# Optimization experiments

Hardware: AMD Instinct MI355X
Metric: run time of the kernel (lower is better)

The kernel has to match this reference:

```python
import jax, jax.numpy as jnp
import numpy as np

B, T, D, H = 4, 4096, 2048, 128

def setup_inputs() -> dict:
    key = jax.random.key(0)
    k1, k2, k3, k4 = jax.random.split(key, 4)
    scale = 0.02
    return {
        "x": jax.random.normal(k1, (B, T, D), dtype=jnp.float32),
        "Wq": jax.random.normal(k2, (D, H), dtype=jnp.float32) * scale,
        "Wk": jax.random.normal(k3, (D, H), dtype=jnp.float32) * scale,
        "Wv": jax.random.normal(k4, (D, H), dtype=jnp.float32) * scale,
    }

def reference(x, Wq, Wk, Wv):
    # x: [B,T,D]; projections to [B,T,H]
    q = jnp.einsum('btd,dh->bth', x, Wq)
    k = jnp.einsum('btd,dh->bth', x, Wk)
    v = jnp.einsum('btd,dh->bth', x, Wv)
    scale = 1.0 / jnp.sqrt(jnp.asarray(q.shape[-1], q.dtype))
    scores = jnp.einsum('bth,bsh->bts', q, k) * scale  # [B,T,T]
    t = x.shape[1]
    causal = jnp.tril(jnp.ones((t, t), dtype=bool))
    scores = jnp.where(causal, scores, -jnp.inf)
    weights = jax.nn.softmax(scores, axis=-1)
    # dropout p=0.0 (eval) -> identity
    out = jnp.einsum('bts,bsh->bth', weights, v)
    return out
```

## Files before the change

### kernel.cpp

```cpp
#include <hip/hip_runtime.h>
#include <hip/hip_bf16.h>

#define Bq 4
#define Tq 4096
#define Dq 2048
#define Hq 128
#define Mq (Bq*Tq)
#define CHUNK 16

typedef __attribute__((ext_vector_type(8))) short bf16x8;
typedef __attribute__((ext_vector_type(4))) float f32x4;

static __device__ __forceinline__ short bfbits(float f) {
    union { __hip_bfloat16 h; short s; } u;
    u.h = __float2bfloat16(f);
    return u.s;
}
static __device__ __forceinline__ float bf2f(short s) {
    union { unsigned u; float f; } v;
    v.u = ((unsigned)(unsigned short)s) << 16;
    return v.f;
}
#define WAIT_LDS() __builtin_amdgcn_s_waitcnt(0xC07F)

static __device__ __forceinline__ void gload16(const void* g, void* l) {
    __builtin_amdgcn_global_load_lds(
        (const __attribute__((address_space(1))) unsigned int*)g,
        (__attribute__((address_space(3))) unsigned int*)l, 16, 0, 0);
}

__global__ __launch_bounds__(256, 1) void wt_kernel(
    const float* __restrict__ Wqp,
    const float* __restrict__ Wkp,
    const float* __restrict__ Wvp,
    short* __restrict__ wTg)
{
    __shared__ short trsp[128][136];
    const int kc = blockIdx.x;
    const int w  = blockIdx.y;
    const float* __restrict__ W = (w == 0) ? Wqp : (w == 1) ? Wkp : Wvp;
    const float scale = (w == 0) ? 0.08838834764831843f : 1.0f;
    const int t = threadIdx.x;

    #pragma unroll
    for (int i = 0; i < 16; i++) {
        int idx = t + i * 256;
        int r = idx >> 5, c4 = idx & 31;
        float4 f = *(const float4*)&W[(size_t)(kc * 128 + r) * Hq + c4 * 4];
        trsp[c4 * 4 + 0][r] = bfbits(f.x * scale);
        trsp[c4 * 4 + 1][r] = bfbits(f.y * scale);
        trsp[c4 * 4 + 2][r] = bfbits(f.z * scale);
        trsp[c4 * 4 + 3][r] = bfbits(f.w * scale);
    }
    __syncthreads();
    #pragma unroll
    for (int i = 0; i < 8; i++) {
        int idx = t + i * 256;
        int h = idx >> 4, c8 = idx & 15;
        *(bf16x8*)&wTg[((size_t)w * 128 + h) * Dq + kc * 128 + c8 * 8] =
            *(bf16x8*)&trsp[h][c8 * 8];
    }
}

__global__ __launch_bounds__(512, 2) void qkv_fused_kernel(
    const float* __restrict__ x,
    const short* __restrict__ wTg,
    short* __restrict__ qg,
    short* __restrict__ kg,
    short* __restrict__ vTt)
{
    __shared__ __attribute__((aligned(128))) char smem[131072];

    const int m0   = blockIdx.x * 64;
    const int t    = threadIdx.x;
    const int l    = t & 63;
    const int w    = t >> 6;
    const int l15  = l & 15;
    const int quad = l >> 4;
    const int wm   = (w >> 2) * 32;
    const int wn   = (w & 3) * 96;

    f32x4 o[2][6];
    #pragma unroll
    for (int mf = 0; mf < 2; mf++)
        #pragma unroll
        for (int j = 0; j < 6; j++) o[mf][j] = (f32x4){0.f, 0.f, 0.f, 0.f};

    const short* wsrcb = wTg + (size_t)(w * 48 + (l >> 3)) * Dq
                             + (((l & 7) ^ ((l >> 3) & 7)) << 3);
    const int xr0 = w * 8 + (l >> 4);

    #define QKV_STAGE(it2, buf)                                                  \
        do {                                                                     \
            const int k0_ = (it2) * 64;                                          \
            char* xb_ = smem + (buf) * 65536;                                    \
            char* wb_ = xb_ + 16384;                                             \
            _Pragma("unroll")                                                    \
            for (int j2 = 0; j2 < 2; j2++) {                                     \
                int r_ = xr0 + j2 * 4;                                           \
                int kbs_ = ((l & 15) ^ (r_ & 15)) << 4;                          \
                gload16((const char*)(x + (size_t)(m0 + r_) * Dq + k0_) + kbs_,  \
                        xb_ + (w * 2 + j2) * 1024);                              \
            }                                                                    \
            _Pragma("unroll")                                                    \
            for (int j = 0; j < 6; j++)                                          \
                gload16(wsrcb + (size_t)j * 8 * Dq + k0_,                        \
                        wb_ + (w * 6 + j) * 1024);                               \
        } while (0)

    QKV_STAGE(0, 0);
    QKV_STAGE(1, 1);

    #pragma unroll 2
    for (int it = 0; it < 32; ++it) {
        if (it < 31) asm volatile("s_waitcnt vmcnt(8)" ::: "memory");
        else         asm volatile("s_waitcnt vmcnt(0)" ::: "memory");
        __builtin_amdgcn_s_barrier();
        __builtin_amdgcn_sched_barrier(0);

        const char* xb = smem + (it & 1) * 65536;
        const char* wb = xb + 16384;
        #pragma unroll
        for (int kk = 0; kk < 2; kk++) {
            bf16x8 a[2];
            #pragma unroll
            for (int mf = 0; mf < 2; mf++) {
                int rm = wm + mf * 16 + l15;
                int sh = (rm & 15) << 4;
                int kb = kk * 128 + quad * 32;
                f32x4 f0 = *(const f32x4*)(xb + rm * 256 + ((kb     ) ^ sh));
                f32x4 f1 = *(const f32x4*)(xb + rm * 256 + ((kb + 16) ^ sh));
                bf16x8 af;
                af[0] = bfbits(f0[0]); af[1] = bfbits(f0[1]);
                af[2] = bfbits(f0[2]); af[3] = bfbits(f0[3]);
                af[4] = bfbits(f1[0]); af[5] = bfbits(f1[1]);
                af[6] = bfbits(f1[2]); af[7] = bfbits(f1[3]);
                a[mf] = af;
            }
            bf16x8 bw[6];
            #pragma unroll
            for (int j = 0; j < 6; j++) {
                int n = wn + j * 16 + l15;
                bw[j] = *(const bf16x8*)(wb + n * 128 +
                        ((kk * 64 + quad * 16) ^ ((n & 7) << 4)));
            }
            #pragma unroll
            for (int mf = 0; mf < 2; mf++)
                #pragma unroll
                for (int j = 0; j < 6; j++)
                    o[mf][j] = __builtin_amdgcn_mfma_f32_16x16x32_bf16(
                        a[mf], bw[j], o[mf][j], 0, 0, 0);
        }

        __builtin_amdgcn_s_barrier();
        __builtin_amdgcn_sched_barrier(0);
        if (it < 30) QKV_STAGE(it + 2, it & 1);
    }
    #undef QKV_STAGE

    {
        short (*e64)[264] = (short(*)[264])smem;
        #pragma unroll
        for (int mf = 0; mf < 2; mf++)
            #pragma unroll
            for (int j = 0; j < 6; j++) {
                int n0 = wn + j * 16;
                if (n0 < 256) {
                    #pragma unroll
                    for (int reg = 0; reg < 4; reg++)
                        e64[wm + mf * 16 + quad * 4 + reg][n0 + l15] = bfbits(o[mf][j][reg]);
                }
            }
        __syncthreads();
        #pragma unroll
        for (int i = 0; i < 4; i++) {
            int idx = t + i * 512;
            int r = idx >> 5, u = idx & 31;
            int n = u * 8;
            bf16x8 val = *(bf16x8*)&e64[r][n];
            short* dst = (n < 128) ? &qg[(size_t)(m0 + r) * Hq + n]
                                   : &kg[(size_t)(m0 + r) * Hq + (n - 128)];
            *(bf16x8*)dst = val;
        }
    }
    __syncthreads();
    {
        short (*e128)[72] = (short(*)[72])smem;
        #pragma unroll
        for (int mf = 0; mf < 2; mf++)
            #pragma unroll
            for (int j = 0; j < 6; j++) {
                int n0 = wn + j * 16;
                if (n0 >= 256) {
                    short4 pk;
                    pk.x = bfbits(o[mf][j][0]); pk.y = bfbits(o[mf][j][1]);
                    pk.z = bfbits(o[mf][j][2]); pk.w = bfbits(o[mf][j][3]);
                    *(short4*)&e128[(n0 - 256) + l15][wm + mf * 16 + quad * 4] = pk;
                }
            }
        __syncthreads();
        const int bb = m0 / Tq;
        const int jt = (m0 % Tq) >> 6;
        #pragma unroll
        for (int i = 0; i < 2; i++) {
            int idx = t + i * 512;
            int h = idx >> 3, u = idx & 7;
            *(bf16x8*)&vTt[(((size_t)bb * (Tq / 64) + jt) * 128 + h) * 64 + u * 8] =
                *(bf16x8*)&e128[h][u * 8];
        }
    }
}

__global__ __launch_bounds__(256, 3) void attn_part_kernel(
    const short* __restrict__ qg, const short* __restrict__ kg,
    const short* __restrict__ vTt,
    short* __restrict__ Opart,
    float* __restrict__ lv)
{
    __shared__ short ks_s[64][136];
    __shared__ short vt_s[128][72];
    __shared__ short ps_s[64][72];

    const int qt = blockIdx.x;
    const int b  = blockIdx.y;
    const int c  = blockIdx.z;
    const int q0 = qt * 64;

    const int lo = c * CHUNK;
    const int hi = min(qt + 1, lo + CHUNK);
    if (lo >= hi) return;

    const int t    = threadIdx.x;
    const int lane = t & 63;
    const int qw   = t >> 6;
    const int l15  = lane & 15;
    const int quad = lane >> 4;

    bf16x8 qf[4];
    {
        const short* qsrc = qg + (size_t)(b * Tq + q0 + qw * 16 + l15) * Hq + quad * 8;
        #pragma unroll
        for (int kk = 0; kk < 4; kk++)
            qf[kk] = *(const bf16x8*)(qsrc + kk * 32);
    }

    float lsum[4] = {0.f, 0.f, 0.f, 0.f};
    f32x4 o[8];
    #pragma unroll
    for (int nf = 0; nf < 8; nf++) o[nf] = (f32x4){0.f, 0.f, 0.f, 0.f};

    bf16x8 kreg[4], vreg[4];
    {
        const size_t kbase = (size_t)(b * Tq + lo * 64) * Hq;
        const short* vsrc = vTt + (((size_t)b * (Tq / 64) + lo) * 128) * 64;
        #pragma unroll
        for (int i = 0; i < 4; i++) {
            int idx = t + i * 256;
            kreg[i] = *(const bf16x8*)&kg[kbase + (size_t)(idx >> 4) * Hq + (idx & 15) * 8];
            vreg[i] = *(const bf16x8*)&vsrc[idx * 8];
        }
        #pragma unroll
        for (int i = 0; i < 4; i++) {
            int idx = t + i * 256;
            *(bf16x8*)&ks_s[idx >> 4][(idx & 15) * 8] = kreg[i];
            *(bf16x8*)&vt_s[idx >> 3][(idx & 7) * 8]  = vreg[i];
        }
    }
    __syncthreads();

    for (int jt = lo; jt < hi; jt++) {
        if (jt + 1 < hi) {
            const size_t kbase = (size_t)(b * Tq + (jt + 1) * 64) * Hq;
            const short* vsrc = vTt + (((size_t)b * (Tq / 64) + jt + 1) * 128) * 64;
            #pragma unroll
            for (int i = 0; i < 4; i++) {
                int idx = t + i * 256;
                kreg[i] = *(const bf16x8*)&kg[kbase + (size_t)(idx >> 4) * Hq + (idx & 15) * 8];
                vreg[i] = *(const bf16x8*)&vsrc[idx * 8];
            }
        }

        f32x4 sacc[4];
        #pragma unroll
        for (int nf = 0; nf < 4; nf++) sacc[nf] = (f32x4){0.f, 0.f, 0.f, 0.f};
        #pragma unroll
        for (int kk = 0; kk < 4; kk++) {
            bf16x8 bk[4];
            #pragma unroll
            for (int nf = 0; nf < 4; nf++)
                bk[nf] = *(bf16x8*)&ks_s[nf * 16 + l15][kk * 32 + quad * 8];
            #pragma unroll
            for (int nf = 0; nf < 4; nf++)
                sacc[nf] = __builtin_amdgcn_mfma_f32_16x16x32_bf16(qf[kk], bk[nf], sacc[nf], 0, 0, 0);
        }

        const bool diag = (jt == qt);
        #pragma unroll
        for (int reg = 0; reg < 4; reg++) {
            const int rloc = qw * 16 + quad * 4 + reg;
            #pragma unroll
            for (int nf = 0; nf < 4; nf++) {
                float s = sacc[nf][reg];
                if (diag && (nf * 16 + l15 > rloc)) s = -1e30f;
                float p = __expf(s);
                lsum[reg] += p;
                ps_s[rloc][nf * 16 + l15] = bfbits(p);
            }
        }
        WAIT_LDS();

        #pragma unroll
        for (int ks2 = 0; ks2 < 2; ks2++) {
            bf16x8 ap = *(bf16x8*)&ps_s[qw * 16 + l15][ks2 * 32 + quad * 8];
            bf16x8 bv[8];
            #pragma unroll
            for (int nf = 0; nf < 8; nf++)
                bv[nf] = *(bf16x8*)&vt_s[nf * 16 + l15][ks2 * 32 + quad * 8];
            #pragma unroll
            for (int nf = 0; nf < 8; nf++)
                o[nf] = __builtin_amdgcn_mfma_f32_16x16x32_bf16(ap, bv[nf], o[nf], 0, 0, 0);
        }

        __syncthreads();
        if (jt + 1 < hi) {
            #pragma unroll
            for (int i = 0; i < 4; i++) {
                int idx = t + i * 256;
                *(bf16x8*)&ks_s[idx >> 4][(idx & 15) * 8] = kreg[i];
                *(bf16x8*)&vt_s[idx >> 3][(idx & 7) * 8]  = vreg[i];
            }
            __syncthreads();
        }
    }

    #pragma unroll
    for (int reg = 0; reg < 4; reg++) {
        #pragma unroll
        for (int mm = 8; mm >= 1; mm >>= 1)
            lsum[reg] += __shfl_xor(lsum[reg], mm, 16);
    }
    const size_t zoff = (size_t)c * Mq;
    if (l15 == 0) {
        #pragma unroll
        for (int reg = 0; reg < 4; reg++)
            lv[zoff + (size_t)b * Tq + q0 + qw * 16 + quad * 4 + reg] = lsum[reg];
    }

    __syncthreads();
    short (*epi)[136] = (short(*)[136])&ks_s[0][0];
    #pragma unroll
    for (int nf = 0; nf < 8; nf++)
        #pragma unroll
        for (int reg = 0; reg < 4; reg++)
            epi[qw * 16 + quad * 4 + reg][nf * 16 + l15] = bfbits(o[nf][reg]);
    __syncthreads();
    #pragma unroll
    for (int i = 0; i < 4; i++) {
        int idx = t + i * 256;
        int r = idx >> 4, cc = idx & 15;
        *(bf16x8*)&Opart[(zoff + (size_t)b * Tq + q0 + r) * Hq + cc * 8] =
            *(bf16x8*)&epi[r][cc * 8];
    }
}

__global__ __launch_bounds__(256, 4) void merge_kernel(
    const short* __restrict__ Opart, const float* __restrict__ lv,
    float* __restrict__ outg)
{
    const int t   = threadIdx.x;
    const int row = blockIdx.x * 16 + (t >> 4);
    const int cu  = t & 15;

    const int rl  = row & (Tq - 1);
    const int nch = (rl >> 10) + 1;

    float lsum = 0.f;
    float acc[8] = {};
    for (int cc = 0; cc < nch; cc++) {
        lsum += lv[(size_t)cc * Mq + row];
        bf16x8 oc = *(const bf16x8*)&Opart[((size_t)cc * Mq + row) * Hq + cu * 8];
        #pragma unroll
        for (int j = 0; j < 8; j++) acc[j] += bf2f(oc[j]);
    }
    float inv = 1.0f / lsum;

    float4 r0, r1;
    r0.x = acc[0] * inv; r0.y = acc[1] * inv; r0.z = acc[2] * inv; r0.w = acc[3] * inv;
    r1.x = acc[4] * inv; r1.y = acc[5] * inv; r1.z = acc[6] * inv; r1.w = acc[7] * inv;
    float* dst = &outg[(size_t)row * Hq + cu * 8];
    *(float4*)dst       = r0;
    *(float4*)(dst + 4) = r1;
}

extern "C" void kernel_launch(void* const* d_in, const int* in_sizes, int n_in,
                              void* d_out, int out_size, void* d_ws, size_t ws_size,
                              hipStream_t stream) {
    const float* x   = (const float*)d_in[0];
    const float* Wqp = (const float*)d_in[1];
    const float* Wkp = (const float*)d_in[2];
    const float* Wvp = (const float*)d_in[3];
    float* out = (float*)d_out;

    short* qg    = (short*)d_ws;
    short* kg    = qg  + (size_t)Mq * Hq;
    short* vTt   = kg  + (size_t)Mq * Hq;
    short* Opart = vTt + (size_t)Mq * Hq;
    short* wTg   = Opart;
    float* lv    = (float*)(Opart + (size_t)4 * Mq * Hq);

    wt_kernel<<<dim3(16, 3), dim3(256), 0, stream>>>(Wqp, Wkp, Wvp, wTg);
    qkv_fused_kernel<<<dim3(Mq / 64), dim3(512), 0, stream>>>(x, wTg, qg, kg, vTt);
    attn_part_kernel<<<dim3(Tq / 64, Bq, 4), dim3(256), 0, stream>>>(qg, kg, vTt, Opart, lv);
    merge_kernel<<<dim3(Mq / 16), dim3(256), 0, stream>>>(Opart, lv, out);
}
```

Baseline: 265.4 us.

## Shrink QKV projection tile to 32 rows with register-staged bf16 x pipeline

The QKV projection kernel now processes 32 rows per block instead of 64, with each of the 8 warps owning 48 output columns. The x tile is loaded into registers, converted to bf16 and written to LDS one step ahead, instead of copying fp32 directly to LDS. A smaller K step (32) and a 52KB LDS footprint allow 4 blocks per CU. The aim is higher occupancy, less LDS traffic for x and better load/compute overlap. The cost is that W tiles are reloaded twice as many times in total and there are more barriers per unit of work.

```diff
diff --git a/kernel.cpp b/kernel.cpp
--- a/kernel.cpp
+++ b/kernel.cpp
@@ -62,118 +62,133 @@
     }
 }
 
-__global__ __launch_bounds__(512, 2) void qkv_fused_kernel(
+__global__ __launch_bounds__(512, 4) void qkv_fused_kernel(
     const float* __restrict__ x,
     const short* __restrict__ wTg,
     short* __restrict__ qg,
     short* __restrict__ kg,
     short* __restrict__ vTt)
 {
-    __shared__ __attribute__((aligned(128))) char smem[131072];
-
-    const int m0   = blockIdx.x * 64;
+    __shared__ __attribute__((aligned(128))) char smem[53248];
+
+    const int m0   = blockIdx.x * 32;
     const int t    = threadIdx.x;
     const int l    = t & 63;
     const int w    = t >> 6;
     const int l15  = l & 15;
     const int quad = l >> 4;
-    const int wm   = (w >> 2) * 32;
-    const int wn   = (w & 3) * 96;
-
-    f32x4 o[2][6];
+    const int wn   = w * 48;
+
+    f32x4 o[2][3];
     #pragma unroll
     for (int mf = 0; mf < 2; mf++)
         #pragma unroll
-        for (int j = 0; j < 6; j++) o[mf][j] = (f32x4){0.f, 0.f, 0.f, 0.f};
-
-    const short* wsrcb = wTg + (size_t)(w * 48 + (l >> 3)) * Dq
-                             + (((l & 7) ^ ((l >> 3) & 7)) << 3);
-    const int xr0 = w * 8 + (l >> 4);
-
-    #define QKV_STAGE(it2, buf)                                                  \
+        for (int j = 0; j < 3; j++) o[mf][j] = (f32x4){0.f, 0.f, 0.f, 0.f};
+
+    const short* wsrc = wTg + (size_t)(w * 48 + (l >> 2)) * Dq + (l & 3) * 8;
+    const int xrow = t >> 4;
+    const float* xsrc = x + (size_t)(m0 + xrow) * Dq + (t & 15) * 2;
+
+    float2 xr0, xr1;
+
+    #define ISSUE_W(it2, buf)                                                    \
         do {                                                                     \
-            const int k0_ = (it2) * 64;                                          \
-            char* xb_ = smem + (buf) * 65536;                                    \
-            char* wb_ = xb_ + 16384;                                             \
+            char* wb_ = smem + (buf) * 26624 + 2048;                             \
             _Pragma("unroll")                                                    \
-            for (int j2 = 0; j2 < 2; j2++) {                                     \
-                int r_ = xr0 + j2 * 4;                                           \
-                int kbs_ = ((l & 15) ^ (r_ & 15)) << 4;                          \
-                gload16((const char*)(x + (size_t)(m0 + r_) * Dq + k0_) + kbs_,  \
-                        xb_ + (w * 2 + j2) * 1024);                              \
-            }                                                                    \
-            _Pragma("unroll")                                                    \
-            for (int j = 0; j < 6; j++)                                          \
-                gload16(wsrcb + (size_t)j * 8 * Dq + k0_,                        \
-                        wb_ + (w * 6 + j) * 1024);                               \
+            for (int j = 0; j < 3; j++)                                          \
+                gload16(wsrc + (size_t)j * 16 * Dq + (it2) * 32,                 \
+                        wb_ + (w * 3 + j) * 1024);                               \
         } while (0)
 
-    QKV_STAGE(0, 0);
-    QKV_STAGE(1, 1);
-
-    #pragma unroll 2
-    for (int it = 0; it < 32; ++it) {
-        if (it < 31) asm volatile("s_waitcnt vmcnt(8)" ::: "memory");
-        else         asm volatile("s_waitcnt vmcnt(0)" ::: "memory");
-        __builtin_amdgcn_s_barrier();
-        __builtin_amdgcn_sched_barrier(0);
-
-        const char* xb = smem + (it & 1) * 65536;
-        const char* wb = xb + 16384;
-        #pragma unroll
-        for (int kk = 0; kk < 2; kk++) {
-            bf16x8 a[2];
-            #pragma unroll
-            for (int mf = 0; mf < 2; mf++) {
-                int rm = wm + mf * 16 + l15;
-                int sh = (rm & 15) << 4;
-                int kb = kk * 128 + quad * 32;
-                f32x4 f0 = *(const f32x4*)(xb + rm * 256 + ((kb     ) ^ sh));
-                f32x4 f1 = *(const f32x4*)(xb + rm * 256 + ((kb + 16) ^ sh));
-                bf16x8 af;
-                af[0] = bfbits(f0[0]); af[1] = bfbits(f0[1]);
-                af[2] = bfbits(f0[2]); af[3] = bfbits(f0[3]);
-                af[4] = bfbits(f1[0]); af[5] = bfbits(f1[1]);
-                af[6] = bfbits(f1[2]); af[7] = bfbits(f1[3]);
-                a[mf] = af;
-            }
-            bf16x8 bw[6];
-            #pragma unroll
-            for (int j = 0; j < 6; j++) {
-                int n = wn + j * 16 + l15;
-                bw[j] = *(const bf16x8*)(wb + n * 128 +
-                        ((kk * 64 + quad * 16) ^ ((n & 7) << 4)));
-            }
-            #pragma unroll
-            for (int mf = 0; mf < 2; mf++)
-                #pragma unroll
-                for (int j = 0; j < 6; j++)
-                    o[mf][j] = __builtin_amdgcn_mfma_f32_16x16x32_bf16(
-                        a[mf], bw[j], o[mf][j], 0, 0, 0);
-        }
-
-        __builtin_amdgcn_s_barrier();
-        __builtin_amdgcn_sched_barrier(0);
-        if (it < 30) QKV_STAGE(it + 2, it & 1);
-    }
-    #undef QKV_STAGE
+    #define WRITE_X(buf, xr)                                                     \
+        do {                                                                     \
+            char* xb_ = smem + (buf) * 26624;                                    \
+            unsigned pk = (unsigned)(unsigned short)bfbits(xr.x)                 \
+                        | ((unsigned)(unsigned short)bfbits(xr.y) << 16);        \
+            *(unsigned*)(xb_ + xrow * 64 + (t & 15) * 4) = pk;                   \
+        } while (0)
+
+    #define COMPUTE(par)                                                         \
+        do {                                                                     \
+            const char* xb_ = smem + (par) * 26624;                              \
+            const char* wb_ = xb_ + 2048;                                        \
+            bf16x8 a0 = *(const bf16x8*)(xb_ + (l15)      * 64 + quad * 16);     \
+            bf16x8 a1 = *(const bf16x8*)(xb_ + (16 + l15) * 64 + quad * 16);     \
+            bf16x8 b0 = *(const bf16x8*)(wb_ + (wn +      l15) * 64 + quad * 16);\
+            bf16x8 b1 = *(const bf16x8*)(wb_ + (wn + 16 + l15) * 64 + quad * 16);\
+            bf16x8 b2 = *(const bf16x8*)(wb_ + (wn + 32 + l15) * 64 + quad * 16);\
+            o[0][0] = __builtin_amdgcn_mfma_f32_16x16x32_bf16(a0, b0, o[0][0], 0, 0, 0); \
+            o[1][0] = __builtin_amdgcn_mfma_f32_16x16x32_bf16(a1, b0, o[1][0], 0, 0, 0); \
+            o[0][1] = __builtin_amdgcn_mfma_f32_16x16x32_bf16(a0, b1, o[0][1], 0, 0, 0); \
+            o[1][1] = __builtin_amdgcn_mfma_f32_16x16x32_bf16(a1, b1, o[1][1], 0, 0, 0); \
+            o[0][2] = __builtin_amdgcn_mfma_f32_16x16x32_bf16(a0, b2, o[0][2], 0, 0, 0); \
+            o[1][2] = __builtin_amdgcn_mfma_f32_16x16x32_bf16(a1, b2, o[1][2], 0, 0, 0); \
+        } while (0)
+
+    #define BODY(it, par, xrNew, xrOld)                                          \
+        do {                                                                     \
+            __builtin_amdgcn_s_barrier();                                        \
+            __builtin_amdgcn_sched_barrier(0);                                   \
+            COMPUTE(par);                                                        \
+            __builtin_amdgcn_s_barrier();                                        \
+            __builtin_amdgcn_sched_barrier(0);                                   \
+            ISSUE_W((it) + 2, par);                                              \
+            xrNew = *(const float2*)(xsrc + ((it) + 2) * 32);                    \
+            asm volatile("s_waitcnt vmcnt(4)" ::: "memory");                     \
+            WRITE_X(1 - (par), xrOld);                                           \
+            asm volatile("s_waitcnt lgkmcnt(0)" ::: "memory");                   \
+            __builtin_amdgcn_sched_barrier(0);                                   \
+        } while (0)
+
+    ISSUE_W(0, 0);
+    xr0 = *(const float2*)(xsrc + 0);
+    ISSUE_W(1, 1);
+    xr1 = *(const float2*)(xsrc + 32);
+    asm volatile("s_waitcnt vmcnt(3)" ::: "memory");
+    WRITE_X(0, xr0);
+    asm volatile("s_waitcnt lgkmcnt(0)" ::: "memory");
+    __builtin_amdgcn_sched_barrier(0);
+
+    #pragma unroll 1
+    for (int itp = 0; itp < 31; itp++) {
+        const int it = itp * 2;
+        BODY(it,     0, xr0, xr1);
+        BODY(it + 1, 1, xr1, xr0);
+    }
+    __builtin_amdgcn_s_barrier();
+    __builtin_amdgcn_sched_barrier(0);
+    COMPUTE(0);
+    __builtin_amdgcn_s_barrier();
+    __builtin_amdgcn_sched_barrier(0);
+    asm volatile("s_waitcnt vmcnt(0)" ::: "memory");
+    WRITE_X(1, xr1);
+    asm volatile("s_waitcnt lgkmcnt(0)" ::: "memory");
+    __builtin_amdgcn_sched_barrier(0);
+    __builtin_amdgcn_s_barrier();
+    COMPUTE(1);
+    __builtin_amdgcn_s_barrier();
+
+    #undef BODY
+    #undef COMPUTE
+    #undef WRITE_X
+    #undef ISSUE_W
 
     {
         short (*e64)[264] = (short(*)[264])smem;
         #pragma unroll
         for (int mf = 0; mf < 2; mf++)
             #pragma unroll
-            for (int j = 0; j < 6; j++) {
+            for (int j = 0; j < 3; j++) {
                 int n0 = wn + j * 16;
                 if (n0 < 256) {
                     #pragma unroll
                     for (int reg = 0; reg < 4; reg++)
-                        e64[wm + mf * 16 + quad * 4 + reg][n0 + l15] = bfbits(o[mf][j][reg]);
+                        e64[mf * 16 + quad * 4 + reg][n0 + l15] = bfbits(o[mf][j][reg]);
                 }
             }
         __syncthreads();
         #pragma unroll
-        for (int i = 0; i < 4; i++) {
+        for (int i = 0; i < 2; i++) {
             int idx = t + i * 512;
             int r = idx >> 5, u = idx & 31;
             int n = u * 8;
@@ -185,27 +200,26 @@
     }
     __syncthreads();
     {
-        short (*e128)[72] = (short(*)[72])smem;
+        short (*e128)[40] = (short(*)[40])smem;
         #pragma unroll
         for (int mf = 0; mf < 2; mf++)
             #pragma unroll
-            for (int j = 0; j < 6; j++) {
+            for (int j = 0; j < 3; j++) {
                 int n0 = wn + j * 16;
                 if (n0 >= 256) {
                     short4 pk;
                     pk.x = bfbits(o[mf][j][0]); pk.y = bfbits(o[mf][j][1]);
                     pk.z = bfbits(o[mf][j][2]); pk.w = bfbits(o[mf][j][3]);
-                    *(short4*)&e128[(n0 - 256) + l15][wm + mf * 16 + quad * 4] = pk;
+                    *(short4*)&e128[(n0 - 256) + l15][mf * 16 + quad * 4] = pk;
                 }
             }
         __syncthreads();
-        const int bb = m0 / Tq;
-        const int jt = (m0 % Tq) >> 6;
-        #pragma unroll
-        for (int i = 0; i < 2; i++) {
-            int idx = t + i * 512;
-            int h = idx >> 3, u = idx & 7;
-            *(bf16x8*)&vTt[(((size_t)bb * (Tq / 64) + jt) * 128 + h) * 64 + u * 8] =
+        const int bb   = m0 / Tq;
+        const int jt   = (m0 % Tq) >> 6;
+        const int moff = m0 & 63;
+        {
+            int h = t >> 2, u = t & 3;
+            *(bf16x8*)&vTt[(((size_t)bb * (Tq / 64) + jt) * 128 + h) * 64 + moff + u * 8] =
                 *(bf16x8*)&e128[h][u * 8];
         }
     }
@@ -409,7 +423,7 @@
     float* lv    = (float*)(Opart + (size_t)4 * Mq * Hq);
 
     wt_kernel<<<dim3(16, 3), dim3(256), 0, stream>>>(Wqp, Wkp, Wvp, wTg);
-    qkv_fused_kernel<<<dim3(Mq / 64), dim3(512), 0, stream>>>(x, wTg, qg, kg, vTt);
+    qkv_fused_kernel<<<dim3(Mq / 32), dim3(512), 0, stream>>>(x, wTg, qg, kg, vTt);
     attn_part_kernel<<<dim3(Tq / 64, Bq, 4), dim3(256), 0, stream>>>(qg, kg, vTt, Opart, lv);
     merge_kernel<<<dim3(Mq / 16), dim3(256), 0, stream>>>(Opart, lv, out);
 }
```

Result: slower. 313.6 us (+18.2%).

## Retile QKV projection into 128x192 output blocks split across N

Applied to the files above, without the earlier changes.

The fused QKV projection moves from 64-row blocks that each compute all 384 output columns to 128-row by 192-column tiles. This gives 256 blocks, one per CU, and each block stages 128 x rows alongside half of the weights. Each fp32 x tile is now read from global memory by two blocks instead of one, and the tile is wider along M to balance the grid. The epilogue is rewritten to route columns to the q, k and transposed-v outputs based on which N half the block owns.

```diff
diff --git a/kernel.cpp b/kernel.cpp
--- a/kernel.cpp
+++ b/kernel.cpp
@@ -69,16 +69,23 @@
     short* __restrict__ kg,
     short* __restrict__ vTt)
 {
-    __shared__ __attribute__((aligned(128))) char smem[131072];
-
-    const int m0   = blockIdx.x * 64;
+    __shared__ __attribute__((aligned(128))) char smem[114688];
+
+    const int bid  = blockIdx.x;
+    const int mi   = bid & 127;
+    const int ni   = bid >> 7;
+    const int m0   = mi * 128;
+    const int n0   = ni * 192;
+
     const int t    = threadIdx.x;
     const int l    = t & 63;
     const int w    = t >> 6;
     const int l15  = l & 15;
     const int quad = l >> 4;
-    const int wm   = (w >> 2) * 32;
-    const int wn   = (w & 3) * 96;
+    const int wmi  = w & 3;
+    const int wni  = w >> 2;
+    const int swzA = l15 << 4;
+    const int swzB = (l15 & 7) << 4;
 
     f32x4 o[2][6];
     #pragma unroll
@@ -86,127 +93,132 @@
         #pragma unroll
         for (int j = 0; j < 6; j++) o[mf][j] = (f32x4){0.f, 0.f, 0.f, 0.f};
 
-    const short* wsrcb = wTg + (size_t)(w * 48 + (l >> 3)) * Dq
-                             + (((l & 7) ^ ((l >> 3) & 7)) << 3);
-    const int xr0 = w * 8 + (l >> 4);
-
-    #define QKV_STAGE(it2, buf)                                                  \
+    const short* wsrc0 = wTg + (size_t)(n0 + 24 * w + (l >> 3)) * Dq
+                             + (((l & 7) ^ (l >> 3)) << 3);
+
+    #define ISSUE(it2, par)                                                      \
         do {                                                                     \
-            const int k0_ = (it2) * 64;                                          \
-            char* xb_ = smem + (buf) * 65536;                                    \
-            char* wb_ = xb_ + 16384;                                             \
+            char* wb_ = smem + (par) * 24576;                                    \
             _Pragma("unroll")                                                    \
-            for (int j2 = 0; j2 < 2; j2++) {                                     \
-                int r_ = xr0 + j2 * 4;                                           \
-                int kbs_ = ((l & 15) ^ (r_ & 15)) << 4;                          \
-                gload16((const char*)(x + (size_t)(m0 + r_) * Dq + k0_) + kbs_,  \
-                        xb_ + (w * 2 + j2) * 1024);                              \
+            for (int j = 0; j < 3; j++)                                          \
+                gload16(wsrc0 + (size_t)j * 8 * Dq + (it2) * 64,                 \
+                        wb_ + (w * 3 + j) * 1024);                               \
+            char* xb_ = smem + 49152 + (par) * 32768;                            \
+            _Pragma("unroll")                                                    \
+            for (int j = 0; j < 4; j++) {                                        \
+                int row_ = 16 * w + 4 * j + (l >> 4);                            \
+                int col_ = ((l & 15) ^ (4 * j + (l >> 4))) << 2;                 \
+                gload16(x + (size_t)(m0 + row_) * Dq + (it2) * 64 + col_,        \
+                        xb_ + (w * 4 + j) * 1024);                               \
             }                                                                    \
+        } while (0)
+
+    #define COMPUTE(par)                                                         \
+        do {                                                                     \
+            const char* wb_ = smem + (par) * 24576;                              \
+            const char* xb_ = smem + 49152 + (par) * 32768;                      \
             _Pragma("unroll")                                                    \
-            for (int j = 0; j < 6; j++)                                          \
-                gload16(wsrcb + (size_t)j * 8 * Dq + k0_,                        \
-                        wb_ + (w * 6 + j) * 1024);                               \
+            for (int kk = 0; kk < 2; kk++) {                                     \
+                bf16x8 a[2], b[6];                                               \
+                _Pragma("unroll")                                                \
+                for (int mf = 0; mf < 2; mf++) {                                 \
+                    const char* rp = xb_ + (wmi * 32 + mf * 16 + l15) * 256;     \
+                    const int kb = kk * 128 + quad * 32;                         \
+                    f32x4 f0 = *(const f32x4*)(rp + ((kb     ) ^ swzA));         \
+                    f32x4 f1 = *(const f32x4*)(rp + ((kb + 16) ^ swzA));         \
+                    bf16x8 af;                                                   \
+                    af[0] = bfbits(f0[0]); af[1] = bfbits(f0[1]);                \
+                    af[2] = bfbits(f0[2]); af[3] = bfbits(f0[3]);                \
+                    af[4] = bfbits(f1[0]); af[5] = bfbits(f1[1]);                \
+                    af[6] = bfbits(f1[2]); af[7] = bfbits(f1[3]);                \
+                    a[mf] = af;                                                  \
+                }                                                                \
+                _Pragma("unroll")                                                \
+                for (int j = 0; j < 6; j++)                                      \
+                    b[j] = *(const bf16x8*)(wb_ + (wni * 96 + j * 16 + l15) * 128\
+                                                + ((kk * 64 + quad * 16) ^ swzB));\
+                _Pragma("unroll")                                                \
+                for (int mf = 0; mf < 2; mf++)                                   \
+                    _Pragma("unroll")                                            \
+                    for (int j = 0; j < 6; j++)                                  \
+                        o[mf][j] = __builtin_amdgcn_mfma_f32_16x16x32_bf16(      \
+                            a[mf], b[j], o[mf][j], 0, 0, 0);                     \
+            }                                                                    \
         } while (0)
 
-    QKV_STAGE(0, 0);
-    QKV_STAGE(1, 1);
-
-    #pragma unroll 2
+    ISSUE(0, 0);
+    ISSUE(1, 1);
+
+    #pragma unroll 1
     for (int it = 0; it < 32; ++it) {
-        if (it < 31) asm volatile("s_waitcnt vmcnt(8)" ::: "memory");
+        if (it < 31) asm volatile("s_waitcnt vmcnt(7)" ::: "memory");
         else         asm volatile("s_waitcnt vmcnt(0)" ::: "memory");
         __builtin_amdgcn_s_barrier();
         __builtin_amdgcn_sched_barrier(0);
-
-        const char* xb = smem + (it & 1) * 65536;
-        const char* wb = xb + 16384;
-        #pragma unroll
-        for (int kk = 0; kk < 2; kk++) {
-            bf16x8 a[2];
-            #pragma unroll
-            for (int mf = 0; mf < 2; mf++) {
-                int rm = wm + mf * 16 + l15;
-                int sh = (rm & 15) << 4;
-                int kb = kk * 128 + quad * 32;
-                f32x4 f0 = *(const f32x4*)(xb + rm * 256 + ((kb     ) ^ sh));
-                f32x4 f1 = *(const f32x4*)(xb + rm * 256 + ((kb + 16) ^ sh));
-                bf16x8 af;
-                af[0] = bfbits(f0[0]); af[1] = bfbits(f0[1]);
-                af[2] = bfbits(f0[2]); af[3] = bfbits(f0[3]);
-                af[4] = bfbits(f1[0]); af[5] = bfbits(f1[1]);
-                af[6] = bfbits(f1[2]); af[7] = bfbits(f1[3]);
-                a[mf] = af;
-            }
-            bf16x8 bw[6];
-            #pragma unroll
-            for (int j = 0; j < 6; j++) {
-                int n = wn + j * 16 + l15;
-                bw[j] = *(const bf16x8*)(wb + n * 128 +
-                        ((kk * 64 + quad * 16) ^ ((n & 7) << 4)));
-            }
-            #pragma unroll
-            for (int mf = 0; mf < 2; mf++)
-                #pragma unroll
-                for (int j = 0; j < 6; j++)
-                    o[mf][j] = __builtin_amdgcn_mfma_f32_16x16x32_bf16(
-                        a[mf], bw[j], o[mf][j], 0, 0, 0);
-        }
-
+        COMPUTE(it & 1);
         __builtin_amdgcn_s_barrier();
         __builtin_amdgcn_sched_barrier(0);
-        if (it < 30) QKV_STAGE(it + 2, it & 1);
-    }
-    #undef QKV_STAGE
+        if (it < 30) ISSUE(it + 2, it & 1);
+    }
+
+    #undef COMPUTE
+    #undef ISSUE
 
     {
-        short (*e64)[264] = (short(*)[264])smem;
+        short (*e)[200] = (short(*)[200])smem;
         #pragma unroll
         for (int mf = 0; mf < 2; mf++)
             #pragma unroll
             for (int j = 0; j < 6; j++) {
-                int n0 = wn + j * 16;
-                if (n0 < 256) {
+                int nloc = wni * 96 + j * 16;
+                if (n0 + nloc < 256) {
                     #pragma unroll
                     for (int reg = 0; reg < 4; reg++)
-                        e64[wm + mf * 16 + quad * 4 + reg][n0 + l15] = bfbits(o[mf][j][reg]);
+                        e[wmi * 32 + mf * 16 + quad * 4 + reg][nloc + l15] =
+                            bfbits(o[mf][j][reg]);
                 }
             }
         __syncthreads();
-        #pragma unroll
-        for (int i = 0; i < 4; i++) {
-            int idx = t + i * 512;
-            int r = idx >> 5, u = idx & 31;
-            int n = u * 8;
-            bf16x8 val = *(bf16x8*)&e64[r][n];
-            short* dst = (n < 128) ? &qg[(size_t)(m0 + r) * Hq + n]
-                                   : &kg[(size_t)(m0 + r) * Hq + (n - 128)];
-            *(bf16x8*)dst = val;
-        }
-    }
-    __syncthreads();
-    {
-        short (*e128)[72] = (short(*)[72])smem;
+        const int r  = t >> 2;
+        const int u0 = (t & 3) * 6;
+        #pragma unroll
+        for (int i = 0; i < 6; i++) {
+            int u  = u0 + i;
+            int ng = n0 + u * 8;
+            if (ng < 256) {
+                bf16x8 val = *(bf16x8*)&e[r][u * 8];
+                short* dst = (ng < 128) ? &qg[(size_t)(m0 + r) * Hq + ng]
+                                        : &kg[(size_t)(m0 + r) * Hq + (ng - 128)];
+                *(bf16x8*)dst = val;
+            }
+        }
+    }
+    if (ni == 1) {
+        __syncthreads();
+        short (*ev)[136] = (short(*)[136])(smem + 53248);
         #pragma unroll
         for (int mf = 0; mf < 2; mf++)
             #pragma unroll
             for (int j = 0; j < 6; j++) {
-                int n0 = wn + j * 16;
-                if (n0 >= 256) {
+                int nloc = wni * 96 + j * 16;
+                if (nloc >= 64) {
                     short4 pk;
                     pk.x = bfbits(o[mf][j][0]); pk.y = bfbits(o[mf][j][1]);
                     pk.z = bfbits(o[mf][j][2]); pk.w = bfbits(o[mf][j][3]);
-                    *(short4*)&e128[(n0 - 256) + l15][wm + mf * 16 + quad * 4] = pk;
+                    *(short4*)&ev[(nloc - 64) + l15][wmi * 32 + mf * 16 + quad * 4] = pk;
                 }
             }
         __syncthreads();
-        const int bb = m0 / Tq;
-        const int jt = (m0 % Tq) >> 6;
-        #pragma unroll
-        for (int i = 0; i < 2; i++) {
+        const int bb  = m0 / Tq;
+        const int jt0 = (m0 % Tq) >> 6;
+        #pragma unroll
+        for (int i = 0; i < 4; i++) {
             int idx = t + i * 512;
-            int h = idx >> 3, u = idx & 7;
-            *(bf16x8*)&vTt[(((size_t)bb * (Tq / 64) + jt) * 128 + h) * 64 + u * 8] =
-                *(bf16x8*)&e128[h][u * 8];
+            int h = idx >> 4, u = idx & 15;
+            int m = u * 8;
+            int jt = jt0 + (m >> 6);
+            *(bf16x8*)&vTt[(((size_t)bb * (Tq / 64) + jt) * 128 + h) * 64 + (m & 63)] =
+                *(bf16x8*)&ev[h][m];
         }
     }
 }
@@ -409,7 +421,7 @@
     float* lv    = (float*)(Opart + (size_t)4 * Mq * Hq);
 
     wt_kernel<<<dim3(16, 3), dim3(256), 0, stream>>>(Wqp, Wkp, Wvp, wTg);
-    qkv_fused_kernel<<<dim3(Mq / 64), dim3(512), 0, stream>>>(x, wTg, qg, kg, vTt);
+    qkv_fused_kernel<<<dim3(256), dim3(512), 0, stream>>>(x, wTg, qg, kg, vTt);
     attn_part_kernel<<<dim3(Tq / 64, Bq, 4), dim3(256), 0, stream>>>(qg, kg, vTt, Opart, lv);
     merge_kernel<<<dim3(Mq / 16), dim3(256), 0, stream>>>(Opart, lv, out);
 }
```

Measured after the change: 265.2 us. About the same (-0.1%).
